# Kernel optimization log

Hardware: AMD Instinct MI355X
Metric: run time of the kernel (lower is better)

## Reference

```python
import jax, jax.numpy as jnp
import numpy as np

N_NODES = 100000
N_EDGES = 3200000
N_IN = 512
N_H = 256

def setup_inputs() -> dict:
    key = jax.random.key(0)
    ks = jax.random.split(key, 8)
    features = jax.random.normal(ks[0], (N_NODES, N_IN), dtype=jnp.float32)
    src = jax.random.randint(ks[1], (N_EDGES,), 0, N_NODES, dtype=jnp.int32)
    dst = jax.random.randint(ks[2], (N_EDGES,), 0, N_NODES, dtype=jnp.int32)
    W1 = jax.random.normal(ks[3], (N_IN, N_H), dtype=jnp.float32) / np.sqrt(N_IN)
    b1 = jnp.zeros((N_H,), dtype=jnp.float32)
    a1 = jnp.full((N_H,), 0.25, dtype=jnp.float32)  # PReLU init
    W2 = jax.random.normal(ks[4], (N_H, N_H), dtype=jnp.float32) / np.sqrt(N_H)
    b2 = jnp.zeros((N_H,), dtype=jnp.float32)
    a2 = jnp.full((N_H,), 0.25, dtype=jnp.float32)
    return {"features": features, "src": src, "dst": dst,
            "W1": W1, "b1": b1, "a1": a1, "W2": W2, "b2": b2, "a2": a2}

def _degree_norms(src, dst, n_nodes):
    ones = jnp.ones(src.shape[0], dtype=jnp.float32)
    out_deg = jax.ops.segment_sum(ones, src, num_segments=n_nodes)
    in_deg = jax.ops.segment_sum(ones, dst, num_segments=n_nodes)
    # DGL clamps degree to min 1 for norm='both'
    norm_src = jax.lax.rsqrt(jnp.maximum(out_deg, 1.0))  # [N]
    norm_dst = jax.lax.rsqrt(jnp.maximum(in_deg, 1.0))   # [N]
    return norm_src, norm_dst

def _graph_conv(x, src, dst, norm_src, norm_dst, W, b, a):
    # DGL GraphConv norm='both': h = Dd^-1/2 * A^T (Ds^-1/2 * x W) + b, then PReLU
    h = (x * norm_src[:, None]) @ W                     # [N, out]
    agg = jax.ops.segment_sum(h[src], dst, num_segments=x.shape[0])  # SpMM gather/scatter
    h = agg * norm_dst[:, None] + b
    return jnp.maximum(h, 0.0) + a * jnp.minimum(h, 0.0)  # PReLU per-channel

def reference(features, src, dst, W1, b1, a1, W2, b2, a2):
    norm_src, norm_dst = _degree_norms(src, dst, features.shape[0])
    h = _graph_conv(features, src, dst, norm_src, norm_dst, W1, b1, a1)
    h = _graph_conv(h, src, dst, norm_src, norm_dst, W2, b2, a2)
    return h
```

## Files before the change

### kernel.cpp

```cpp
#include <hip/hip_runtime.h>
#include <hip/hip_bf16.h>

typedef unsigned short u16;
typedef short s16x8 __attribute__((ext_vector_type(8)));
typedef u16 u16x4 __attribute__((ext_vector_type(4)));
typedef u16 u16x8 __attribute__((ext_vector_type(8)));
typedef float f32x4 __attribute__((ext_vector_type(4)));

#define BSHIFT 10

__device__ __forceinline__ u16 f2bf(float f) {
    __hip_bfloat16 b = __float2bfloat16(f);
    return __builtin_bit_cast(u16, b);
}
__device__ __forceinline__ float bf2f(u16 u) {
    unsigned int x = ((unsigned int)u) << 16;
    return __builtin_bit_cast(float, x);
}


__global__ __launch_bounds__(256) void bhist_k(const int* __restrict__ src,
                                               const int* __restrict__ dst,
                                               int* __restrict__ bcntA,
                                               int* __restrict__ bcntB,
                                               int E, int chunk) {
    __shared__ int hA[128], hB[128];
    const int base = blockIdx.x * chunk;
    const int end = (base + chunk) < E ? (base + chunk) : E;
    if (threadIdx.x < 128) { hA[threadIdx.x] = 0; hB[threadIdx.x] = 0; }
    __syncthreads();
    for (int i = base + threadIdx.x; i < end; i += 256) {
        atomicAdd(&hA[dst[i] >> BSHIFT], 1);
        atomicAdd(&hB[src[i] >> BSHIFT], 1);
    }
    __syncthreads();
    if (threadIdx.x < 128) {
        if (hA[threadIdx.x]) atomicAdd(&bcntA[threadIdx.x], hA[threadIdx.x]);
        if (hB[threadIdx.x]) atomicAdd(&bcntB[threadIdx.x], hB[threadIdx.x]);
    }
}

__global__ void bscan_k(const int* __restrict__ bcntA, const int* __restrict__ bcntB,
                        int* __restrict__ bbaseA, int* __restrict__ bbaseB,
                        int* __restrict__ bcurA, int* __restrict__ bcurB,
                        int* __restrict__ row_ptr, int NB, int N, int E) {
    __shared__ int tA[128], tB[128];
    const int t = threadIdx.x;
    int vA = (t < NB) ? bcntA[t] : 0;
    int vB = (t < NB) ? bcntB[t] : 0;
    tA[t] = vA; tB[t] = vB;
    __syncthreads();
    for (int d = 1; d < 128; d <<= 1) {
        int aA = (t >= d) ? tA[t - d] : 0;
        int aB = (t >= d) ? tB[t - d] : 0;
        __syncthreads();
        tA[t] += aA; tB[t] += aB;
        __syncthreads();
    }
    if (t < NB) {
        int eA = tA[t] - vA, eB = tB[t] - vB;
        bbaseA[t] = eA; bcurA[t] = eA;
        bbaseB[t] = eB; bcurB[t] = eB;
    } else if (t == NB) {
        bbaseA[NB] = E; bbaseB[NB] = E;
    }
    if (t == 0) row_ptr[N] = E;
}

__global__ __launch_bounds__(256) void part_k(const int* __restrict__ src,
                                              const int* __restrict__ dst,
                                              int* __restrict__ bcurA,
                                              int* __restrict__ bcurB,
                                              int2* __restrict__ pairs,
                                              int* __restrict__ sb,
                                              int E, int chunk) {
    __shared__ int hA[128], hB[128];
    const int base = blockIdx.x * chunk;
    const int end = (base + chunk) < E ? (base + chunk) : E;
    if (threadIdx.x < 128) { hA[threadIdx.x] = 0; hB[threadIdx.x] = 0; }
    __syncthreads();
    for (int i = base + threadIdx.x; i < end; i += 256) {
        atomicAdd(&hA[dst[i] >> BSHIFT], 1);
        atomicAdd(&hB[src[i] >> BSHIFT], 1);
    }
    __syncthreads();
    if (threadIdx.x < 128) {
        int c = hA[threadIdx.x];
        hA[threadIdx.x] = c ? atomicAdd(&bcurA[threadIdx.x], c) : 0;
        c = hB[threadIdx.x];
        hB[threadIdx.x] = c ? atomicAdd(&bcurB[threadIdx.x], c) : 0;
    }
    __syncthreads();
    for (int i = base + threadIdx.x; i < end; i += 256) {
        int d = dst[i], s = src[i];
        int posA = atomicAdd(&hA[d >> BSHIFT], 1);
        int2 pr; pr.x = s; pr.y = d;
        pairs[posA] = pr;
        int posB = atomicAdd(&hB[s >> BSHIFT], 1);
        sb[posB] = s;
    }
}

__global__ __launch_bounds__(256) void bcsr_k(const int2* __restrict__ pairs,
                                              const int* __restrict__ bbase,
                                              int* __restrict__ row_ptr,
                                              int* __restrict__ din,
                                              int* __restrict__ col, int N) {
    __shared__ int hist[1024];
    __shared__ int cur[1024];
    __shared__ int psum[256];
    const int b = blockIdx.x;
    const int beg = bbase[b], end = bbase[b + 1];
    const int nbase = b << BSHIFT;
    const int nlen = (N - nbase) < 1024 ? (N - nbase) : 1024;
    const int t = threadIdx.x;
#pragma unroll
    for (int j = 0; j < 4; j++) hist[t * 4 + j] = 0;
    __syncthreads();
    for (int i = beg + t; i < end; i += 256)
        atomicAdd(&hist[pairs[i].y - nbase], 1);
    __syncthreads();
    int h0 = hist[4 * t], h1 = hist[4 * t + 1], h2 = hist[4 * t + 2], h3 = hist[4 * t + 3];
    int s = h0 + h1 + h2 + h3;
    psum[t] = s;
    __syncthreads();
    for (int d = 1; d < 256; d <<= 1) {
        int add = (t >= d) ? psum[t - d] : 0;
        __syncthreads();
        psum[t] += add;
        __syncthreads();
    }
    int e0 = psum[t] - s;
    int e1 = e0 + h0, e2 = e1 + h1, e3 = e2 + h2;
    cur[4 * t] = beg + e0; cur[4 * t + 1] = beg + e1;
    cur[4 * t + 2] = beg + e2; cur[4 * t + 3] = beg + e3;
    if (4 * t + 0 < nlen) { row_ptr[nbase + 4 * t + 0] = beg + e0; din[nbase + 4 * t + 0] = h0; }
    if (4 * t + 1 < nlen) { row_ptr[nbase + 4 * t + 1] = beg + e1; din[nbase + 4 * t + 1] = h1; }
    if (4 * t + 2 < nlen) { row_ptr[nbase + 4 * t + 2] = beg + e2; din[nbase + 4 * t + 2] = h2; }
    if (4 * t + 3 < nlen) { row_ptr[nbase + 4 * t + 3] = beg + e3; din[nbase + 4 * t + 3] = h3; }
    __syncthreads();
    for (int i = beg + t; i < end; i += 256) {
        int2 p = pairs[i];
        int pos = atomicAdd(&cur[p.y - nbase], 1);
        col[pos] = p.x;
    }
}

__global__ __launch_bounds__(256) void bdeg_k(const int* __restrict__ sb,
                                              const int* __restrict__ bbase,
                                              int* __restrict__ dout, int N) {
    __shared__ int hist[1024];
    const int b = blockIdx.x;
    const int beg = bbase[b], end = bbase[b + 1];
    const int nbase = b << BSHIFT;
    const int nlen = (N - nbase) < 1024 ? (N - nbase) : 1024;
    for (int i = threadIdx.x; i < 1024; i += 256) hist[i] = 0;
    __syncthreads();
    for (int i = beg + threadIdx.x; i < end; i += 256)
        atomicAdd(&hist[sb[i] - nbase], 1);
    __syncthreads();
    for (int i = threadIdx.x; i < nlen; i += 256) dout[nbase + i] = hist[i];
}

__global__ __launch_bounds__(256) void sortrow_k(const int* __restrict__ rp,
                                                 int* __restrict__ col, int n) {
    int w = (blockIdx.x * blockDim.x + threadIdx.x) >> 6;
    if (w >= n) return;
    const int lane = threadIdx.x & 63;
    const int beg = rp[w], end = rp[w + 1];
    const int deg = end - beg;
    if (deg <= 1) return;
    if (deg <= 128) {
        const int INF = 0x7fffffff;
        int a = (lane < deg) ? col[beg + lane] : INF;
        int b = (64 + lane < deg) ? col[beg + 64 + lane] : INF;
#pragma unroll
        for (int k = 2; k <= 128; k <<= 1) {
#pragma unroll
            for (int j = k >> 1; j > 0; j >>= 1) {
                if (j >= 64) {
                    int lo = a < b ? a : b, hi = a < b ? b : a;
                    a = lo; b = hi;
                } else {
                    int pa = __shfl_xor(a, j);
                    int pb = __shfl_xor(b, j);
                    bool lower = ((lane & j) == 0);
                    bool asc_a = ((lane & k) == 0);
                    bool asc_b = (((lane + 64) & k) == 0);
                    int mna = a < pa ? a : pa, mxa = a < pa ? pa : a;
                    int mnb = b < pb ? b : pb, mxb = b < pb ? pb : b;
                    a = (lower == asc_a) ? mna : mxa;
                    b = (lower == asc_b) ? mnb : mxb;
                }
            }
        }
        if (lane < deg) col[beg + lane] = a;
        if (64 + lane < deg) col[beg + 64 + lane] = b;
    } else if (lane == 0) {
        for (int i = beg + 1; i < end; i++) {
            int v = col[i], j = i - 1;
            while (j >= beg && col[j] > v) { col[j + 1] = col[j]; j--; }
            col[j + 1] = v;
        }
    }
}

__global__ void norms_k(const int* __restrict__ dout, const int* __restrict__ din,
                        float* __restrict__ ns, float* __restrict__ nd, int n) {
    int i = blockIdx.x * blockDim.x + threadIdx.x;
    if (i < n) {
        ns[i] = 1.0f / sqrtf(fmaxf((float)dout[i], 1.0f));
        nd[i] = 1.0f / sqrtf(fmaxf((float)din[i], 1.0f));
    }
}

__global__ void convt_k(const float* __restrict__ W, u16* __restrict__ Wt, int K, int Nn) {
    int i = blockIdx.x * blockDim.x + threadIdx.x;
    if (i < K * Nn) {
        int n = i / K, k = i - n * K;
        Wt[i] = f2bf(W[(size_t)k * Nn + n]);
    }
}


template <int K, bool AF32>
__global__ __launch_bounds__(512) void gemm_k(const void* __restrict__ Ap,
                                              const float* __restrict__ nsrc,
                                              const u16* __restrict__ Bt,
                                              u16* __restrict__ C, int M) {
    constexpr int BKt = 64;
    __shared__ u16 Al[128 * BKt];
    __shared__ u16 Bl[256 * BKt];
    const int tid = threadIdx.x, lane = tid & 63, wid = tid >> 6;
    const int wr = wid >> 2, wc = wid & 3;
    const int l15 = lane & 15, lhi = lane >> 4;
    const int bm = blockIdx.x * 128;
    f32x4 acc[4][4] = {};

    for (int k0 = 0; k0 < K; k0 += BKt) {
#pragma unroll
        for (int i = 0; i < 2; i++) {
            int G = i * 512 + tid, row = G >> 3, gk = G & 7;
            int grow = bm + row;
            grow = grow < M ? grow : M - 1;
            u16x8 w;
            if constexpr (AF32) {
                const float* A = (const float*)Ap;
                const f32x4 v0 = *(const f32x4*)(A + (size_t)grow * K + k0 + gk * 8);
                const f32x4 v1 = *(const f32x4*)(A + (size_t)grow * K + k0 + gk * 8 + 4);
                const float ns = nsrc[grow];
                w[0] = f2bf(v0[0] * ns); w[1] = f2bf(v0[1] * ns);
                w[2] = f2bf(v0[2] * ns); w[3] = f2bf(v0[3] * ns);
                w[4] = f2bf(v1[0] * ns); w[5] = f2bf(v1[1] * ns);
                w[6] = f2bf(v1[2] * ns); w[7] = f2bf(v1[3] * ns);
            } else {
                const u16* A = (const u16*)Ap;
                w = *(const u16x8*)(A + (size_t)grow * K + k0 + gk * 8);
            }
            int idx = (row * BKt + gk * 8) ^ ((row & 7) << 3);
            *(u16x8*)(Al + idx) = w;
        }
#pragma unroll
        for (int i = 0; i < 4; i++) {
            int G = i * 512 + tid, row = G >> 3, gk = G & 7;
            u16x8 wb = *(const u16x8*)(Bt + (size_t)row * K + k0 + gk * 8);
            int idx = (row * BKt + gk * 8) ^ ((row & 7) << 3);
            *(u16x8*)(Bl + idx) = wb;
        }
        __syncthreads();

        s16x8 af[2][4], bfr[2][4];
#pragma unroll
        for (int kk = 0; kk < 2; kk++) {
#pragma unroll
            for (int mi = 0; mi < 4; mi++) {
                int row = wr * 64 + mi * 16 + l15;
                int idx = (row * BKt + kk * 32 + lhi * 8) ^ ((row & 7) << 3);
                af[kk][mi] = *(const s16x8*)(Al + idx);
            }
#pragma unroll
            for (int ni = 0; ni < 4; ni++) {
                int n = wc * 64 + ni * 16 + l15;
                int idx = (n * BKt + kk * 32 + lhi * 8) ^ ((n & 7) << 3);
                bfr[kk][ni] = *(const s16x8*)(Bl + idx);
            }
        }
#pragma unroll
        for (int kk = 0; kk < 2; kk++)
#pragma unroll
            for (int mi = 0; mi < 4; mi++)
#pragma unroll
                for (int ni = 0; ni < 4; ni++)
                    acc[mi][ni] = __builtin_amdgcn_mfma_f32_16x16x32_bf16(
                        af[kk][mi], bfr[kk][ni], acc[mi][ni], 0, 0, 0);
        __syncthreads();
    }

#pragma unroll
    for (int mi = 0; mi < 4; mi++) {
#pragma unroll
        for (int r = 0; r < 4; r++) {
            int grow = bm + wr * 64 + mi * 16 + lhi * 4 + r;
            if (grow < M) {
#pragma unroll
                for (int ni = 0; ni < 4; ni++) {
                    int gcol = wc * 64 + ni * 16 + l15;
                    C[(size_t)grow * 256 + gcol] = f2bf(acc[mi][ni][r]);
                }
            }
        }
    }
}


__global__ __launch_bounds__(256, 4) void agg_k(const u16* __restrict__ h,
                                                const int* __restrict__ rp,
                                                const int* __restrict__ col,
                                                const float* __restrict__ nd,
                                                const float* __restrict__ bias,
                                                const float* __restrict__ alpha,
                                                const float* __restrict__ ns,
                                                u16* __restrict__ obf, float* __restrict__ of,
                                                int n) {
    int w = (blockIdx.x * blockDim.x + threadIdx.x) >> 5;
    if (w >= n) return;
    const int c0 = (threadIdx.x & 31) * 8;
    const int beg = rp[w], end = rp[w + 1];
    const u16* __restrict__ hb = h + c0;

    float a0[8] = {}, a1[8] = {}, a2[8] = {}, a3[8] = {};

    int p = beg;
    if (p + 7 < end) {
        int s0 = col[p], s1 = col[p + 1], s2 = col[p + 2], s3 = col[p + 3];
        int s4 = col[p + 4], s5 = col[p + 5], s6 = col[p + 6], s7 = col[p + 7];
        while (true) {
            u16x8 v0 = *(const u16x8*)(hb + (size_t)s0 * 256);
            u16x8 v1 = *(const u16x8*)(hb + (size_t)s1 * 256);
            u16x8 v2 = *(const u16x8*)(hb + (size_t)s2 * 256);
            u16x8 v3 = *(const u16x8*)(hb + (size_t)s3 * 256);
            u16x8 v4 = *(const u16x8*)(hb + (size_t)s4 * 256);
            u16x8 v5 = *(const u16x8*)(hb + (size_t)s5 * 256);
            u16x8 v6 = *(const u16x8*)(hb + (size_t)s6 * 256);
            u16x8 v7 = *(const u16x8*)(hb + (size_t)s7 * 256);
            p += 8;
            bool more = (p + 7 < end);
            if (more) {
                s0 = col[p]; s1 = col[p + 1]; s2 = col[p + 2]; s3 = col[p + 3];
                s4 = col[p + 4]; s5 = col[p + 5]; s6 = col[p + 6]; s7 = col[p + 7];
            }
#pragma unroll
            for (int j = 0; j < 8; j++) {
                a0[j] += bf2f(v0[j]);
                a1[j] += bf2f(v1[j]);
                a2[j] += bf2f(v2[j]);
                a3[j] += bf2f(v3[j]);
            }
#pragma unroll
            for (int j = 0; j < 8; j++) {
                a0[j] += bf2f(v4[j]);
                a1[j] += bf2f(v5[j]);
                a2[j] += bf2f(v6[j]);
                a3[j] += bf2f(v7[j]);
            }
            if (!more) break;
        }
    }
    for (; p + 3 < end; p += 4) {
        int s0 = col[p], s1 = col[p + 1], s2 = col[p + 2], s3 = col[p + 3];
        u16x8 v0 = *(const u16x8*)(hb + (size_t)s0 * 256);
        u16x8 v1 = *(const u16x8*)(hb + (size_t)s1 * 256);
        u16x8 v2 = *(const u16x8*)(hb + (size_t)s2 * 256);
        u16x8 v3 = *(const u16x8*)(hb + (size_t)s3 * 256);
#pragma unroll
        for (int j = 0; j < 8; j++) {
            a0[j] += bf2f(v0[j]);
            a1[j] += bf2f(v1[j]);
            a2[j] += bf2f(v2[j]);
            a3[j] += bf2f(v3[j]);
        }
    }
    for (; p < end; p++) {
        int s = col[p];
        u16x8 v = *(const u16x8*)(hb + (size_t)s * 256);
#pragma unroll
        for (int j = 0; j < 8; j++) a0[j] += bf2f(v[j]);
    }
#pragma unroll
    for (int j = 0; j < 8; j++) a0[j] = (a0[j] + a1[j]) + (a2[j] + a3[j]);

    const float ndv = nd[w];
    const f32x4 bv0 = *(const f32x4*)(bias + c0);
    const f32x4 bv1 = *(const f32x4*)(bias + c0 + 4);
    const f32x4 al0 = *(const f32x4*)(alpha + c0);
    const f32x4 al1 = *(const f32x4*)(alpha + c0 + 4);
    float bb[8] = {bv0[0], bv0[1], bv0[2], bv0[3], bv1[0], bv1[1], bv1[2], bv1[3]};
    float aa[8] = {al0[0], al0[1], al0[2], al0[3], al1[0], al1[1], al1[2], al1[3]};
#pragma unroll
    for (int j = 0; j < 8; j++) {
        float s = a0[j] * ndv + bb[j];
        a0[j] = s > 0.f ? s : aa[j] * s;
    }

    if (obf) {
        const float nsv = ns[w];
        u16x8 o;
#pragma unroll
        for (int j = 0; j < 8; j++) o[j] = f2bf(a0[j] * nsv);
        *(u16x8*)(obf + (size_t)w * 256 + c0) = o;
    } else {
        f32x4 o0, o1;
        o0[0] = a0[0]; o0[1] = a0[1]; o0[2] = a0[2]; o0[3] = a0[3];
        o1[0] = a0[4]; o1[1] = a0[5]; o1[2] = a0[6]; o1[3] = a0[7];
        *(f32x4*)(of + (size_t)w * 256 + c0) = o0;
        *(f32x4*)(of + (size_t)w * 256 + c0 + 4) = o1;
    }
}


extern "C" void kernel_launch(void* const* d_in, const int* in_sizes, int n_in,
                              void* d_out, int out_size, void* d_ws, size_t ws_size,
                              hipStream_t stream) {
    const float* feat = (const float*)d_in[0];
    const int* src = (const int*)d_in[1];
    const int* dst = (const int*)d_in[2];
    const float* W1 = (const float*)d_in[3];
    const float* b1 = (const float*)d_in[4];
    const float* a1 = (const float*)d_in[5];
    const float* W2 = (const float*)d_in[6];
    const float* b2 = (const float*)d_in[7];
    const float* a2 = (const float*)d_in[8];
    float* out = (float*)d_out;

    const int N = in_sizes[0] / 512;
    const int E = in_sizes[1];
    const int NB = (N + (1 << BSHIFT) - 1) >> BSHIFT;

    char* ws = (char*)d_ws;
    size_t off = 0;
    auto take = [&](size_t bytes) {
        size_t o = off;
        off += (bytes + 255) & ~(size_t)255;
        return o;
    };
    int* deg_out = (int*)(ws + take((size_t)N * 4));
    int* deg_in = (int*)(ws + take((size_t)N * 4));
    float* nsrc = (float*)(ws + take((size_t)N * 4));
    float* ndst = (float*)(ws + take((size_t)N * 4));
    int* row_ptr = (int*)(ws + take((size_t)(N + 1) * 4));
    int* bcnt = (int*)(ws + take(1024));
    int* bcntA = bcnt, * bcntB = bcnt + 128;
    int* bbaseA = (int*)(ws + take(512));
    int* bbaseB = (int*)(ws + take(512));
    int* bcurA = (int*)(ws + take(512));
    int* bcurB = (int*)(ws + take(512));
    int* col = (int*)(ws + take((size_t)E * 4));
    u16* W1t = (u16*)(ws + take((size_t)512 * 256 * 2));
    u16* W2t = (u16*)(ws + take((size_t)256 * 256 * 2));
    u16* h = (u16*)(ws + take((size_t)N * 256 * 2));
    u16* x2 = (u16*)(ws + take((size_t)N * 256 * 2));
    int2* pairs = (int2*)h;
    int* sb = (int*)x2;

    hipMemsetAsync(bcnt, 0, 1024, stream);

    const int chunk = 4096;
    bhist_k<<<(E + chunk - 1) / chunk, 256, 0, stream>>>(src, dst, bcntA, bcntB, E, chunk);
    bscan_k<<<1, 128, 0, stream>>>(bcntA, bcntB, bbaseA, bbaseB, bcurA, bcurB, row_ptr, NB, N, E);
    part_k<<<(E + chunk - 1) / chunk, 256, 0, stream>>>(src, dst, bcurA, bcurB, pairs, sb, E, chunk);
    bcsr_k<<<NB, 256, 0, stream>>>(pairs, bbaseA, row_ptr, deg_in, col, N);
    bdeg_k<<<NB, 256, 0, stream>>>(sb, bbaseB, deg_out, N);
    sortrow_k<<<(N * 64 + 255) / 256, 256, 0, stream>>>(row_ptr, col, N);
    norms_k<<<(N + 255) / 256, 256, 0, stream>>>(deg_out, deg_in, nsrc, ndst, N);

    convt_k<<<(512 * 256 + 255) / 256, 256, 0, stream>>>(W1, W1t, 512, 256);
    convt_k<<<(256 * 256 + 255) / 256, 256, 0, stream>>>(W2, W2t, 256, 256);

    dim3 gg((N + 127) / 128);
    int aggBlocks = (N * 32 + 255) / 256;

    gemm_k<512, true><<<gg, 512, 0, stream>>>(feat, nsrc, W1t, h, N);
    agg_k<<<aggBlocks, 256, 0, stream>>>(h, row_ptr, col, ndst, b1, a1, nsrc, x2, nullptr, N);
    gemm_k<256, false><<<gg, 512, 0, stream>>>(x2, nullptr, W2t, h, N);
    agg_k<<<aggBlocks, 256, 0, stream>>>(h, row_ptr, col, ndst, b2, a2, nullptr, nullptr, out, N);
}
```

Before: 825.6 us.

## Pipeline SpMM neighbor gathers through LDS with async global_load_lds ring

Rewrites the aggregation kernel so each 64-lane wave handles two nodes, stages their column indices in shared memory, and streams neighbor rows into an 8-deep per-wave LDS ring using asynchronous global-to-LDS loads with vmcnt waits. This keeps several gathers in flight without holding them in registers, replacing the register-unrolled 4-accumulator loop. The risks are divergence when the two paired nodes have different degrees (padding loads to index 0), LDS capacity limiting occupancy, and reliance on hand-coded waitcnt values being correct.

After: 860.1 us. 4.2% more time.

```diff
diff --git a/kernel.cpp b/kernel.cpp
--- a/kernel.cpp
+++ b/kernel.cpp
@@ -8,6 +8,7 @@
 typedef float f32x4 __attribute__((ext_vector_type(4)));
 
 #define BSHIFT 10
+#define AGG_D 8
 
 __device__ __forceinline__ u16 f2bf(float f) {
     __hip_bfloat16 b = __float2bfloat16(f);
@@ -16,6 +17,11 @@
 __device__ __forceinline__ float bf2f(u16 u) {
     unsigned int x = ((unsigned int)u) << 16;
     return __builtin_bit_cast(float, x);
+}
+
+__device__ __forceinline__ void gload_lds16(const u16* g, u16* l) {
+    __builtin_amdgcn_global_load_lds((const __attribute__((address_space(1))) void*)g,
+                                     (__attribute__((address_space(3))) void*)l, 16, 0, 0);
 }
 
 
@@ -313,83 +319,97 @@
 }
 
 
-__global__ __launch_bounds__(256, 4) void agg_k(const u16* __restrict__ h,
-                                                const int* __restrict__ rp,
-                                                const int* __restrict__ col,
-                                                const float* __restrict__ nd,
-                                                const float* __restrict__ bias,
-                                                const float* __restrict__ alpha,
-                                                const float* __restrict__ ns,
-                                                u16* __restrict__ obf, float* __restrict__ of,
-                                                int n) {
-    int w = (blockIdx.x * blockDim.x + threadIdx.x) >> 5;
-    if (w >= n) return;
-    const int c0 = (threadIdx.x & 31) * 8;
-    const int beg = rp[w], end = rp[w + 1];
-    const u16* __restrict__ hb = h + c0;
-
-    float a0[8] = {}, a1[8] = {}, a2[8] = {}, a3[8] = {};
-
-    int p = beg;
-    if (p + 7 < end) {
-        int s0 = col[p], s1 = col[p + 1], s2 = col[p + 2], s3 = col[p + 3];
-        int s4 = col[p + 4], s5 = col[p + 5], s6 = col[p + 6], s7 = col[p + 7];
-        while (true) {
-            u16x8 v0 = *(const u16x8*)(hb + (size_t)s0 * 256);
-            u16x8 v1 = *(const u16x8*)(hb + (size_t)s1 * 256);
-            u16x8 v2 = *(const u16x8*)(hb + (size_t)s2 * 256);
-            u16x8 v3 = *(const u16x8*)(hb + (size_t)s3 * 256);
-            u16x8 v4 = *(const u16x8*)(hb + (size_t)s4 * 256);
-            u16x8 v5 = *(const u16x8*)(hb + (size_t)s5 * 256);
-            u16x8 v6 = *(const u16x8*)(hb + (size_t)s6 * 256);
-            u16x8 v7 = *(const u16x8*)(hb + (size_t)s7 * 256);
-            p += 8;
-            bool more = (p + 7 < end);
-            if (more) {
-                s0 = col[p]; s1 = col[p + 1]; s2 = col[p + 2]; s3 = col[p + 3];
-                s4 = col[p + 4]; s5 = col[p + 5]; s6 = col[p + 6]; s7 = col[p + 7];
-            }
-#pragma unroll
-            for (int j = 0; j < 8; j++) {
-                a0[j] += bf2f(v0[j]);
-                a1[j] += bf2f(v1[j]);
-                a2[j] += bf2f(v2[j]);
-                a3[j] += bf2f(v3[j]);
-            }
-#pragma unroll
-            for (int j = 0; j < 8; j++) {
-                a0[j] += bf2f(v4[j]);
-                a1[j] += bf2f(v5[j]);
-                a2[j] += bf2f(v6[j]);
-                a3[j] += bf2f(v7[j]);
-            }
-            if (!more) break;
-        }
-    }
-    for (; p + 3 < end; p += 4) {
-        int s0 = col[p], s1 = col[p + 1], s2 = col[p + 2], s3 = col[p + 3];
-        u16x8 v0 = *(const u16x8*)(hb + (size_t)s0 * 256);
-        u16x8 v1 = *(const u16x8*)(hb + (size_t)s1 * 256);
-        u16x8 v2 = *(const u16x8*)(hb + (size_t)s2 * 256);
-        u16x8 v3 = *(const u16x8*)(hb + (size_t)s3 * 256);
-#pragma unroll
-        for (int j = 0; j < 8; j++) {
-            a0[j] += bf2f(v0[j]);
-            a1[j] += bf2f(v1[j]);
-            a2[j] += bf2f(v2[j]);
-            a3[j] += bf2f(v3[j]);
-        }
-    }
-    for (; p < end; p++) {
-        int s = col[p];
-        u16x8 v = *(const u16x8*)(hb + (size_t)s * 256);
-#pragma unroll
-        for (int j = 0; j < 8; j++) a0[j] += bf2f(v[j]);
-    }
-#pragma unroll
-    for (int j = 0; j < 8; j++) a0[j] = (a0[j] + a1[j]) + (a2[j] + a3[j]);
-
-    const float ndv = nd[w];
+__global__ __launch_bounds__(256) void agg_k(const u16* __restrict__ h,
+                                             const int* __restrict__ rp,
+                                             const int* __restrict__ col,
+                                             const float* __restrict__ nd,
+                                             const float* __restrict__ bias,
+                                             const float* __restrict__ alpha,
+                                             const float* __restrict__ ns,
+                                             u16* __restrict__ obf, float* __restrict__ of,
+                                             int n) {
+    __shared__ u16 stage[4][AGG_D][512];
+    __shared__ int colbuf[4][256];
+    const int tid = threadIdx.x;
+    const int wid = tid >> 6, lane = tid & 63;
+    const int q = blockIdx.x * 4 + wid;
+    const int half = lane >> 5, l31 = lane & 31;
+    const int node = 2 * q + half;
+
+    int myBeg = 0, myDeg = 0;
+    if (node < n) { myBeg = rp[node]; myDeg = rp[node + 1] - myBeg; }
+    const int degA = __shfl(myDeg, 0);
+    const int degB = __shfl(myDeg, 32);
+    const int begA = __shfl(myBeg, 0);
+    const int begB = __shfl(myBeg, 32);
+    const int km = degA > degB ? degA : degB;
+
+    float a[8] = {};
+    const u16* hb = h + l31 * 8;
+
+    if (km > 0 && km <= 128) {
+        const int tot = degA + degB;
+        for (int i = lane; i < tot; i += 64) {
+            int v = (i < degA) ? col[begA + i] : col[begB + (i - degA)];
+            int slot = (i < degA) ? i : (128 + i - degA);
+            colbuf[wid][slot] = v;
+        }
+        const int cbase = half << 7;
+        if (km <= AGG_D) {
+            for (int k = 0; k < km; ++k) {
+                if (k < myDeg) {
+                    int s = colbuf[wid][cbase + k];
+                    u16x8 v = *(const u16x8*)(hb + (size_t)s * 256);
+#pragma unroll
+                    for (int j = 0; j < 8; j++) a[j] += bf2f(v[j]);
+                }
+            }
+        } else {
+            __builtin_amdgcn_s_waitcnt(0x0F70);
+#pragma unroll
+            for (int k = 0; k < AGG_D; ++k) {
+                int s = (k < myDeg) ? colbuf[wid][cbase + k] : 0;
+                gload_lds16(hb + (size_t)s * 256, &stage[wid][k][0]);
+            }
+            for (int c = 0; c < km - AGG_D; ++c) {
+                __builtin_amdgcn_s_waitcnt(0x0F77);
+                __builtin_amdgcn_sched_barrier(0);
+                const int slot = c & (AGG_D - 1);
+                u16x8 v = *(const u16x8*)&stage[wid][slot][lane * 8];
+#pragma unroll
+                for (int j = 0; j < 8; j++) {
+                    float x = (c < myDeg) ? bf2f(v[j]) : 0.f;
+                    a[j] += x;
+                }
+                __builtin_amdgcn_sched_barrier(0);
+                const int k = c + AGG_D;
+                int s = (k < myDeg) ? colbuf[wid][cbase + k] : 0;
+                gload_lds16(hb + (size_t)s * 256, &stage[wid][slot][0]);
+            }
+            __builtin_amdgcn_s_waitcnt(0x0F70);
+            __builtin_amdgcn_sched_barrier(0);
+            for (int c = km - AGG_D; c < km; ++c) {
+                const int slot = c & (AGG_D - 1);
+                u16x8 v = *(const u16x8*)&stage[wid][slot][lane * 8];
+#pragma unroll
+                for (int j = 0; j < 8; j++) {
+                    float x = (c < myDeg) ? bf2f(v[j]) : 0.f;
+                    a[j] += x;
+                }
+            }
+        }
+    } else if (km > 128) {
+        for (int k = 0; k < myDeg; ++k) {
+            int s = col[myBeg + k];
+            u16x8 v = *(const u16x8*)(hb + (size_t)s * 256);
+#pragma unroll
+            for (int j = 0; j < 8; j++) a[j] += bf2f(v[j]);
+        }
+    }
+
+    if (node >= n) return;
+    const int c0 = l31 * 8;
+    const float ndv = nd[node];
     const f32x4 bv0 = *(const f32x4*)(bias + c0);
     const f32x4 bv1 = *(const f32x4*)(bias + c0 + 4);
     const f32x4 al0 = *(const f32x4*)(alpha + c0);
@@ -398,22 +418,22 @@
     float aa[8] = {al0[0], al0[1], al0[2], al0[3], al1[0], al1[1], al1[2], al1[3]};
 #pragma unroll
     for (int j = 0; j < 8; j++) {
-        float s = a0[j] * ndv + bb[j];
-        a0[j] = s > 0.f ? s : aa[j] * s;
+        float s = a[j] * ndv + bb[j];
+        a[j] = s > 0.f ? s : aa[j] * s;
     }
 
     if (obf) {
-        const float nsv = ns[w];
+        const float nsv = ns[node];
         u16x8 o;
 #pragma unroll
-        for (int j = 0; j < 8; j++) o[j] = f2bf(a0[j] * nsv);
-        *(u16x8*)(obf + (size_t)w * 256 + c0) = o;
+        for (int j = 0; j < 8; j++) o[j] = f2bf(a[j] * nsv);
+        *(u16x8*)(obf + (size_t)node * 256 + c0) = o;
     } else {
         f32x4 o0, o1;
-        o0[0] = a0[0]; o0[1] = a0[1]; o0[2] = a0[2]; o0[3] = a0[3];
-        o1[0] = a0[4]; o1[1] = a0[5]; o1[2] = a0[6]; o1[3] = a0[7];
-        *(f32x4*)(of + (size_t)w * 256 + c0) = o0;
-        *(f32x4*)(of + (size_t)w * 256 + c0 + 4) = o1;
+        o0[0] = a[0]; o0[1] = a[1]; o0[2] = a[2]; o0[3] = a[3];
+        o1[0] = a[4]; o1[1] = a[5]; o1[2] = a[6]; o1[3] = a[7];
+        *(f32x4*)(of + (size_t)node * 256 + c0) = o0;
+        *(f32x4*)(of + (size_t)node * 256 + c0 + 4) = o1;
     }
 }
 
@@ -477,7 +497,8 @@
     convt_k<<<(256 * 256 + 255) / 256, 256, 0, stream>>>(W2, W2t, 256, 256);
 
     dim3 gg((N + 127) / 128);
-    int aggBlocks = (N * 32 + 255) / 256;
+    const int numPairs = (N + 1) / 2;
+    const int aggBlocks = (numPairs + 3) / 4;
 
     gemm_k<512, true><<<gg, 512, 0, stream>>>(feat, nsrc, W1t, h, N);
     agg_k<<<aggBlocks, 256, 0, stream>>>(h, row_ptr, col, ndst, b1, a1, nsrc, x2, nullptr, N);
```

## Pack edge pairs into one int key and simplify aggregation loop

Applied to the files above, without the earlier changes.

The partition step now packs each edge into a single 32-bit code, holding the source index shifted left plus the low 10 bits of the destination, instead of an int2 pair. This halves the scratch traffic written by part_k and read twice by bcsr_k. The aggregation kernel drops its software-pipelined index prefetch in favour of a plain 8-wide unrolled loop and removes the occupancy hint from launch_bounds. The packing relies on the source index fitting in 22 bits, and the simpler loop may expose more latency on col loads.

Result: no change. 815.6 us (-1.2%).

```diff
diff --git a/kernel.cpp b/kernel.cpp
--- a/kernel.cpp
+++ b/kernel.cpp
@@ -3,7 +3,6 @@
 
 typedef unsigned short u16;
 typedef short s16x8 __attribute__((ext_vector_type(8)));
-typedef u16 u16x4 __attribute__((ext_vector_type(4)));
 typedef u16 u16x8 __attribute__((ext_vector_type(8)));
 typedef float f32x4 __attribute__((ext_vector_type(4)));
 
@@ -71,7 +70,7 @@
                                               const int* __restrict__ dst,
                                               int* __restrict__ bcurA,
                                               int* __restrict__ bcurB,
-                                              int2* __restrict__ pairs,
+                                              int* __restrict__ kcode,
                                               int* __restrict__ sb,
                                               int E, int chunk) {
     __shared__ int hA[128], hB[128];
@@ -94,14 +93,13 @@
     for (int i = base + threadIdx.x; i < end; i += 256) {
         int d = dst[i], s = src[i];
         int posA = atomicAdd(&hA[d >> BSHIFT], 1);
-        int2 pr; pr.x = s; pr.y = d;
-        pairs[posA] = pr;
+        kcode[posA] = (s << BSHIFT) | (d & 1023);
         int posB = atomicAdd(&hB[s >> BSHIFT], 1);
         sb[posB] = s;
     }
 }
 
-__global__ __launch_bounds__(256) void bcsr_k(const int2* __restrict__ pairs,
+__global__ __launch_bounds__(256) void bcsr_k(const int* __restrict__ kcode,
                                               const int* __restrict__ bbase,
                                               int* __restrict__ row_ptr,
                                               int* __restrict__ din,
@@ -118,7 +116,7 @@
     for (int j = 0; j < 4; j++) hist[t * 4 + j] = 0;
     __syncthreads();
     for (int i = beg + t; i < end; i += 256)
-        atomicAdd(&hist[pairs[i].y - nbase], 1);
+        atomicAdd(&hist[kcode[i] & 1023], 1);
     __syncthreads();
     int h0 = hist[4 * t], h1 = hist[4 * t + 1], h2 = hist[4 * t + 2], h3 = hist[4 * t + 3];
     int s = h0 + h1 + h2 + h3;
@@ -140,9 +138,9 @@
     if (4 * t + 3 < nlen) { row_ptr[nbase + 4 * t + 3] = beg + e3; din[nbase + 4 * t + 3] = h3; }
     __syncthreads();
     for (int i = beg + t; i < end; i += 256) {
-        int2 p = pairs[i];
-        int pos = atomicAdd(&cur[p.y - nbase], 1);
-        col[pos] = p.x;
+        int k = kcode[i];
+        int pos = atomicAdd(&cur[k & 1023], 1);
+        col[pos] = k >> BSHIFT;
     }
 }
 
@@ -313,65 +311,34 @@
 }
 
 
-__global__ __launch_bounds__(256, 4) void agg_k(const u16* __restrict__ h,
-                                                const int* __restrict__ rp,
-                                                const int* __restrict__ col,
-                                                const float* __restrict__ nd,
-                                                const float* __restrict__ bias,
-                                                const float* __restrict__ alpha,
-                                                const float* __restrict__ ns,
-                                                u16* __restrict__ obf, float* __restrict__ of,
-                                                int n) {
+__global__ __launch_bounds__(256) void agg_k(const u16* __restrict__ h,
+                                             const int* __restrict__ rp,
+                                             const int* __restrict__ col,
+                                             const float* __restrict__ nd,
+                                             const float* __restrict__ bias,
+                                             const float* __restrict__ alpha,
+                                             const float* __restrict__ ns,
+                                             u16* __restrict__ obf, float* __restrict__ of,
+                                             int n) {
     int w = (blockIdx.x * blockDim.x + threadIdx.x) >> 5;
     if (w >= n) return;
     const int c0 = (threadIdx.x & 31) * 8;
     const int beg = rp[w], end = rp[w + 1];
-    const u16* __restrict__ hb = h + c0;
 
     float a0[8] = {}, a1[8] = {}, a2[8] = {}, a3[8] = {};
 
     int p = beg;
-    if (p + 7 < end) {
+    for (; p + 7 < end; p += 8) {
         int s0 = col[p], s1 = col[p + 1], s2 = col[p + 2], s3 = col[p + 3];
         int s4 = col[p + 4], s5 = col[p + 5], s6 = col[p + 6], s7 = col[p + 7];
-        while (true) {
-            u16x8 v0 = *(const u16x8*)(hb + (size_t)s0 * 256);
-            u16x8 v1 = *(const u16x8*)(hb + (size_t)s1 * 256);
-            u16x8 v2 = *(const u16x8*)(hb + (size_t)s2 * 256);
-            u16x8 v3 = *(const u16x8*)(hb + (size_t)s3 * 256);
-            u16x8 v4 = *(const u16x8*)(hb + (size_t)s4 * 256);
-            u16x8 v5 = *(const u16x8*)(hb + (size_t)s5 * 256);
-            u16x8 v6 = *(const u16x8*)(hb + (size_t)s6 * 256);
-            u16x8 v7 = *(const u16x8*)(hb + (size_t)s7 * 256);
-            p += 8;
-            bool more = (p + 7 < end);
-            if (more) {
-                s0 = col[p]; s1 = col[p + 1]; s2 = col[p + 2]; s3 = col[p + 3];
-                s4 = col[p + 4]; s5 = col[p + 5]; s6 = col[p + 6]; s7 = col[p + 7];
-            }
-#pragma unroll
-            for (int j = 0; j < 8; j++) {
-                a0[j] += bf2f(v0[j]);
-                a1[j] += bf2f(v1[j]);
-                a2[j] += bf2f(v2[j]);
-                a3[j] += bf2f(v3[j]);
-            }
-#pragma unroll
-            for (int j = 0; j < 8; j++) {
-                a0[j] += bf2f(v4[j]);
-                a1[j] += bf2f(v5[j]);
-                a2[j] += bf2f(v6[j]);
-                a3[j] += bf2f(v7[j]);
-            }
-            if (!more) break;
-        }
-    }
-    for (; p + 3 < end; p += 4) {
-        int s0 = col[p], s1 = col[p + 1], s2 = col[p + 2], s3 = col[p + 3];
-        u16x8 v0 = *(const u16x8*)(hb + (size_t)s0 * 256);
-        u16x8 v1 = *(const u16x8*)(hb + (size_t)s1 * 256);
-        u16x8 v2 = *(const u16x8*)(hb + (size_t)s2 * 256);
-        u16x8 v3 = *(const u16x8*)(hb + (size_t)s3 * 256);
+        u16x8 v0 = *(const u16x8*)(h + (size_t)s0 * 256 + c0);
+        u16x8 v1 = *(const u16x8*)(h + (size_t)s1 * 256 + c0);
+        u16x8 v2 = *(const u16x8*)(h + (size_t)s2 * 256 + c0);
+        u16x8 v3 = *(const u16x8*)(h + (size_t)s3 * 256 + c0);
+        u16x8 v4 = *(const u16x8*)(h + (size_t)s4 * 256 + c0);
+        u16x8 v5 = *(const u16x8*)(h + (size_t)s5 * 256 + c0);
+        u16x8 v6 = *(const u16x8*)(h + (size_t)s6 * 256 + c0);
+        u16x8 v7 = *(const u16x8*)(h + (size_t)s7 * 256 + c0);
 #pragma unroll
         for (int j = 0; j < 8; j++) {
             a0[j] += bf2f(v0[j]);
@@ -379,10 +346,31 @@
             a2[j] += bf2f(v2[j]);
             a3[j] += bf2f(v3[j]);
         }
+#pragma unroll
+        for (int j = 0; j < 8; j++) {
+            a0[j] += bf2f(v4[j]);
+            a1[j] += bf2f(v5[j]);
+            a2[j] += bf2f(v6[j]);
+            a3[j] += bf2f(v7[j]);
+        }
+    }
+    for (; p + 3 < end; p += 4) {
+        int s0 = col[p], s1 = col[p + 1], s2 = col[p + 2], s3 = col[p + 3];
+        u16x8 v0 = *(const u16x8*)(h + (size_t)s0 * 256 + c0);
+        u16x8 v1 = *(const u16x8*)(h + (size_t)s1 * 256 + c0);
+        u16x8 v2 = *(const u16x8*)(h + (size_t)s2 * 256 + c0);
+        u16x8 v3 = *(const u16x8*)(h + (size_t)s3 * 256 + c0);
+#pragma unroll
+        for (int j = 0; j < 8; j++) {
+            a0[j] += bf2f(v0[j]);
+            a1[j] += bf2f(v1[j]);
+            a2[j] += bf2f(v2[j]);
+            a3[j] += bf2f(v3[j]);
+        }
     }
     for (; p < end; p++) {
         int s = col[p];
-        u16x8 v = *(const u16x8*)(hb + (size_t)s * 256);
+        u16x8 v = *(const u16x8*)(h + (size_t)s * 256 + c0);
 #pragma unroll
         for (int j = 0; j < 8; j++) a0[j] += bf2f(v[j]);
     }
@@ -459,7 +447,7 @@
     u16* W2t = (u16*)(ws + take((size_t)256 * 256 * 2));
     u16* h = (u16*)(ws + take((size_t)N * 256 * 2));
     u16* x2 = (u16*)(ws + take((size_t)N * 256 * 2));
-    int2* pairs = (int2*)h;
+    int* kcode = (int*)h;
     int* sb = (int*)x2;
 
     hipMemsetAsync(bcnt, 0, 1024, stream);
@@ -467,8 +455,8 @@
     const int chunk = 4096;
     bhist_k<<<(E + chunk - 1) / chunk, 256, 0, stream>>>(src, dst, bcntA, bcntB, E, chunk);
     bscan_k<<<1, 128, 0, stream>>>(bcntA, bcntB, bbaseA, bbaseB, bcurA, bcurB, row_ptr, NB, N, E);
-    part_k<<<(E + chunk - 1) / chunk, 256, 0, stream>>>(src, dst, bcurA, bcurB, pairs, sb, E, chunk);
-    bcsr_k<<<NB, 256, 0, stream>>>(pairs, bbaseA, row_ptr, deg_in, col, N);
+    part_k<<<(E + chunk - 1) / chunk, 256, 0, stream>>>(src, dst, bcurA, bcurB, kcode, sb, E, chunk);
+    bcsr_k<<<NB, 256, 0, stream>>>(kcode, bbaseA, row_ptr, deg_in, col, N);
     bdeg_k<<<NB, 256, 0, stream>>>(sb, bbaseB, deg_out, N);
     sortrow_k<<<(N * 64 + 255) / 256, 256, 0, stream>>>(row_ptr, col, N);
     norms_k<<<(N + 255) / 256, 256, 0, stream>>>(deg_out, deg_in, nsrc, ndst, N);
```
